# Performance work log

Measured on AMD Instinct MI355X. Metric: run time of the kernel, lower is better.

## Reference

```python
import jax, jax.numpy as jnp
import numpy as np

# GraphConvolutionSparse forward:
#   x = sparse_dropout(X)            (dropout=0.0 -> identity, kept faithful)
#   h = X @ W                        (sparse-dense matmul via segment_sum)
#   h = A @ h                        (sparse-dense matmul via segment_sum)
#   out = relu(h)

DROPOUT = 0.0  # layer default; keep_prob = 1 - dropout

def setup_inputs() -> dict:
    key = jax.random.key(0)
    k1, k2, k3, k4, k5, k6, k7 = jax.random.split(key, 7)
    N = 100000       # nodes
    D_IN = 512       # input feature dim
    D_OUT = 128      # output feature dim
    NNZ_X = 800000   # nonzeros in sparse feature matrix
    N_E = 1600000    # adjacency nonzeros (edges)
    x_vals = jax.random.normal(k1, (NNZ_X,), dtype=jnp.float32)
    x_rows = jax.random.randint(k2, (NNZ_X,), 0, N, dtype=jnp.int32)
    x_cols = jax.random.randint(k3, (NNZ_X,), 0, D_IN, dtype=jnp.int32)
    adj_vals = jax.random.uniform(k4, (N_E,), dtype=jnp.float32)
    adj_rows = jax.random.randint(k5, (N_E,), 0, N, dtype=jnp.int32)
    adj_cols = jax.random.randint(k6, (N_E,), 0, N, dtype=jnp.int32)
    init_range = np.sqrt(6.0 / (D_IN + D_OUT)).astype(np.float32)
    W = jax.random.uniform(k7, (D_IN, D_OUT), minval=-init_range, maxval=init_range, dtype=jnp.float32)
    return {"x_vals": x_vals, "x_rows": x_rows, "x_cols": x_cols,
            "adj_vals": adj_vals, "adj_rows": adj_rows, "adj_cols": adj_cols,
            "W": W, "n_nodes": N}

def reference(x_vals, x_rows, x_cols, adj_vals, adj_rows, adj_cols, W, n_nodes):
    keep_prob = 1.0 - DROPOUT
    # sparse dropout: with dropout=0.0 the mask keeps all entries and scale is 1,
    # so it reduces to the deterministic identity (faithful to tf semantics).
    vals = x_vals * (1.0 / keep_prob)
    # h = X @ W : gather weight rows by feature column, scale, scatter-add by node row
    xw = jax.ops.segment_sum(vals[:, None] * W[x_cols], x_rows, num_segments=n_nodes)  # [N, D_OUT]
    # out = A @ h : gather source-node rows, scale by edge weight, scatter-add to dest
    agg = jax.ops.segment_sum(adj_vals[:, None] * xw[adj_cols], adj_rows, num_segments=n_nodes)  # [N, D_OUT]
    return jax.nn.relu(agg)
```

## Files before the change

kernel.cpp:

```cpp
#include <hip/hip_runtime.h>
#include <hip/hip_fp16.h>


#define DOUT 128
#define RB 32
#define RB_BITS 5
#define NBMAX 4096
#define CAPL 1024
#define COLMASK 131071
#define CTH 256
#define CWAVES 4
#define CAPX 448
#define CAPA 768

static inline size_t align_up(size_t x, size_t a) { return (x + a - 1) & ~(a - 1); }

__device__ inline int wave_incl_scan(int v, int lane) {
    #pragma unroll
    for (int off = 1; off < 64; off <<= 1) {
        int up = __shfl_up(v, off, 64);
        if (lane >= off) v += up;
    }
    return v;
}

__global__ __launch_bounds__(256) void prep_kernel(int* __restrict__ cnts, int ncnt,
                                                   const float* __restrict__ W,
                                                   __half2* __restrict__ Wh, int whtot) {
    int i = blockIdx.x * 256 + threadIdx.x;
    if (i < ncnt) cnts[i] = 0;
    if (i < whtot) {
        int c = i >> 6, l = i & 63;
        Wh[i] = __floats2half2_rn(W[(c << 7) + 2 * l], W[(c << 7) + 2 * l + 1]);
    }
}

__global__ __launch_bounds__(256) void hist_coarse(const int* __restrict__ xr, int nx,
                                                   const int* __restrict__ ar, int na,
                                                   int* __restrict__ cx, int* __restrict__ ca) {
    __shared__ int h[2 * NBMAX];
    for (int i = threadIdx.x; i < 2 * NBMAX; i += 256) h[i] = 0;
    __syncthreads();
    int base = blockIdx.x * 4096;
    int tot = nx + na;
    #pragma unroll
    for (int k = 0; k < 16; ++k) {
        int i = base + k * 256 + threadIdx.x;
        if (i < tot) {
            if (i < nx) atomicAdd(&h[xr[i] >> RB_BITS], 1);
            else        atomicAdd(&h[NBMAX + (ar[i - nx] >> RB_BITS)], 1);
        }
    }
    __syncthreads();
    for (int i = threadIdx.x; i < 2 * NBMAX; i += 256) {
        int c = h[i];
        if (c) {
            if (i < NBMAX) atomicAdd(&cx[i], c);
            else           atomicAdd(&ca[i - NBMAX], c);
        }
    }
}

__global__ __launch_bounds__(1024) void scan_nb(const int* __restrict__ cx, const int* __restrict__ ca,
                                                int* __restrict__ bx, int* __restrict__ ba,
                                                int* __restrict__ curx, int* __restrict__ cura, int nb) {
    const int* c = blockIdx.x ? ca : cx;
    int* bs  = blockIdx.x ? ba : bx;
    int* cur = blockIdx.x ? cura : curx;
    __shared__ int wsum[16];
    __shared__ int woff[16];
    __shared__ int carry_s, chunk_tot;
    int tid = threadIdx.x, lane = tid & 63, wid = tid >> 6;
    if (tid == 0) carry_s = 0;
    __syncthreads();
    for (int base = 0; base < nb; base += 1024) {
        int i = base + tid;
        int v = (i < nb) ? c[i] : 0;
        int incl = wave_incl_scan(v, lane);
        if (lane == 63) wsum[wid] = incl;
        __syncthreads();
        if (wid == 0 && lane < 16) {
            int s = wsum[lane];
            int is = s;
            #pragma unroll
            for (int off = 1; off < 16; off <<= 1) {
                int up = __shfl_up(is, off, 64);
                if (lane >= off) is += up;
            }
            woff[lane] = is - s;
            if (lane == 15) chunk_tot = is;
        }
        __syncthreads();
        int excl = incl - v + woff[wid] + carry_s;
        if (i < nb) { bs[i] = excl; cur[i] = excl; }
        __syncthreads();
        if (tid == 0) carry_s += chunk_tot;
        __syncthreads();
    }
    if (tid == 0) bs[nb] = carry_s;
}

__global__ __launch_bounds__(512) void bucket_scatter2(const int* __restrict__ xr, const int* __restrict__ xc,
                                                       const float* __restrict__ xv, int nx,
                                                       const int* __restrict__ ar, const int* __restrict__ ac,
                                                       const float* __restrict__ av, int na,
                                                       int* __restrict__ curx, int* __restrict__ cura,
                                                       int2* __restrict__ stx, int2* __restrict__ sta,
                                                       int nb, int nblk_x, int capx, int capa) {
    const int* rows; const int* cols; const float* vals; int n;
    int* gcur; int2* stage; int base; int cap;
    if (blockIdx.x < nblk_x) {
        rows = xr; cols = xc; vals = xv; n = nx; gcur = curx; stage = stx;
        base = blockIdx.x * 4096; cap = capx;
    } else {
        rows = ar; cols = ac; vals = av; n = na; gcur = cura; stage = sta;
        base = (blockIdx.x - nblk_x) * 4096; cap = capa;
    }
    __shared__ int h[NBMAX];
    __shared__ int bcur[NBMAX];
    for (int i = threadIdx.x; i < nb; i += 512) h[i] = 0;
    __syncthreads();
    int rr[8]; int cc[8]; float vv[8];
    #pragma unroll
    for (int k = 0; k < 8; ++k) {
        int i = base + k * 512 + threadIdx.x;
        rr[k] = -1;
        if (i < n) {
            rr[k] = rows[i]; cc[k] = cols[i]; vv[k] = vals[i];
            atomicAdd(&h[rr[k] >> RB_BITS], 1);
        }
    }
    __syncthreads();
    for (int b = threadIdx.x; b < nb; b += 512) {
        int c = h[b];
        if (c) {
            int r = atomicAdd(&gcur[b], c);
            bcur[b] = (cap > 0) ? (b * cap + r) : r;
        }
    }
    __syncthreads();
    #pragma unroll
    for (int k = 0; k < 8; ++k) {
        if (rr[k] >= 0) {
            int b = rr[k] >> RB_BITS;
            int p = atomicAdd(&bcur[b], 1);
            if (cap == 0 || p < b * cap + cap)
                stage[p] = make_int2(((rr[k] & (RB - 1)) << 17) | cc[k], __float_as_int(vv[k]));
        }
    }
}


__global__ __launch_bounds__(CTH) void consumer_xw(const int* __restrict__ bx, const int* __restrict__ gcnt,
                                                   const int2* __restrict__ stage,
                                                   const __half2* __restrict__ Wh, __half2* __restrict__ xwh,
                                                   int N, int cap) {
    __shared__ int2 sp[CAPL];
    __shared__ int hoff[RB + 1];
    __shared__ int curs[RB];
    int b = blockIdx.x;
    int s, cnt;
    if (cap > 0) { s = b * cap; cnt = min(gcnt[b], cap); }
    else         { s = bx[b]; cnt = bx[b + 1] - s; }
    int tid = threadIdx.x, lane = tid & 63, wid = tid >> 6;
    bool fast = (cnt <= CAPL);
    if (tid < RB) curs[tid] = 0;
    __syncthreads();
    if (fast) {
        for (int i = tid; i < cnt; i += CTH)
            atomicAdd(&curs[(stage[s + i].x >> 17) & (RB - 1)], 1);
    }
    __syncthreads();
    if (wid == 0) {
        int v = (lane < RB) ? curs[lane] : 0;
        int incl = wave_incl_scan(v, lane);
        if (lane < RB) {
            int excl = incl - v;
            hoff[lane] = excl;
            curs[lane] = excl;
            if (lane == RB - 1) hoff[RB] = incl;
        }
    }
    __syncthreads();
    if (fast) {
        for (int i = tid; i < cnt; i += CTH) {
            int2 p = stage[s + i];
            int r = (p.x >> 17) & (RB - 1);
            sp[atomicAdd(&curs[r], 1)] = p;
        }
    }
    __syncthreads();
    int row0 = b << RB_BITS;
    #pragma unroll 1
    for (int rr = 0; rr < RB / CWAVES; ++rr) {
        int r = wid + rr * CWAVES;
        int grow = row0 + r;
        if (grow >= N) continue;
        float ax = 0.f, ay = 0.f;
        if (fast) {
            int j = hoff[r], o1 = hoff[r + 1];
            for (; j + 3 < o1; j += 4) {
                int2 c0 = sp[j], c1 = sp[j + 1], c2 = sp[j + 2], c3 = sp[j + 3];
                float2 w0 = __half22float2(Wh[((size_t)(c0.x & COLMASK) << 6) + lane]);
                float2 w1 = __half22float2(Wh[((size_t)(c1.x & COLMASK) << 6) + lane]);
                float2 w2 = __half22float2(Wh[((size_t)(c2.x & COLMASK) << 6) + lane]);
                float2 w3 = __half22float2(Wh[((size_t)(c3.x & COLMASK) << 6) + lane]);
                float v0 = __int_as_float(c0.y), v1 = __int_as_float(c1.y);
                float v2 = __int_as_float(c2.y), v3 = __int_as_float(c3.y);
                ax += v0 * w0.x + v1 * w1.x + v2 * w2.x + v3 * w3.x;
                ay += v0 * w0.y + v1 * w1.y + v2 * w2.y + v3 * w3.y;
            }
            for (; j < o1; ++j) {
                int2 c0 = sp[j];
                float2 w0 = __half22float2(Wh[((size_t)(c0.x & COLMASK) << 6) + lane]);
                float v0 = __int_as_float(c0.y);
                ax += v0 * w0.x; ay += v0 * w0.y;
            }
        } else {
            for (int j = 0; j < cnt; ++j) {
                int2 c0 = stage[s + j];
                if (((c0.x >> 17) & (RB - 1)) == r) {
                    float2 w0 = __half22float2(Wh[((size_t)(c0.x & COLMASK) << 6) + lane]);
                    float v0 = __int_as_float(c0.y);
                    ax += v0 * w0.x; ay += v0 * w0.y;
                }
            }
        }
        xwh[((size_t)grow << 6) + lane] = __float22half2_rn(make_float2(ax, ay));
    }
}

__global__ __launch_bounds__(CTH) void consumer_adj(const int* __restrict__ ba, const int* __restrict__ gcnt,
                                                    const int2* __restrict__ stage,
                                                    const __half2* __restrict__ xwh, float* __restrict__ out,
                                                    int N, int cap) {
    __shared__ int2 sp[CAPL];
    __shared__ int hoff[RB + 1];
    __shared__ int curs[RB];
    int b = blockIdx.x;
    int s, cnt;
    if (cap > 0) { s = b * cap; cnt = min(gcnt[b], cap); }
    else         { s = ba[b]; cnt = ba[b + 1] - s; }
    int tid = threadIdx.x, lane = tid & 63, wid = tid >> 6;
    bool fast = (cnt <= CAPL);
    if (tid < RB) curs[tid] = 0;
    __syncthreads();
    if (fast) {
        for (int i = tid; i < cnt; i += CTH)
            atomicAdd(&curs[(stage[s + i].x >> 17) & (RB - 1)], 1);
    }
    __syncthreads();
    if (wid == 0) {
        int v = (lane < RB) ? curs[lane] : 0;
        int incl = wave_incl_scan(v, lane);
        if (lane < RB) {
            int excl = incl - v;
            hoff[lane] = excl;
            curs[lane] = excl;
            if (lane == RB - 1) hoff[RB] = incl;
        }
    }
    __syncthreads();
    if (fast) {
        for (int i = tid; i < cnt; i += CTH) {
            int2 p = stage[s + i];
            int r = (p.x >> 17) & (RB - 1);
            sp[atomicAdd(&curs[r], 1)] = p;
        }
    }
    __syncthreads();
    int row0 = b << RB_BITS;
    #pragma unroll 1
    for (int rr = 0; rr < RB / CWAVES; ++rr) {
        int r = wid + rr * CWAVES;
        int grow = row0 + r;
        if (grow >= N) continue;
        float ax = 0.f, ay = 0.f;
        if (fast) {
            int j = hoff[r], o1 = hoff[r + 1];
            for (; j + 3 < o1; j += 4) {
                int2 c0 = sp[j], c1 = sp[j + 1], c2 = sp[j + 2], c3 = sp[j + 3];
                float2 h0 = __half22float2(xwh[((size_t)(c0.x & COLMASK) << 6) + lane]);
                float2 h1 = __half22float2(xwh[((size_t)(c1.x & COLMASK) << 6) + lane]);
                float2 h2 = __half22float2(xwh[((size_t)(c2.x & COLMASK) << 6) + lane]);
                float2 h3 = __half22float2(xwh[((size_t)(c3.x & COLMASK) << 6) + lane]);
                float v0 = __int_as_float(c0.y), v1 = __int_as_float(c1.y);
                float v2 = __int_as_float(c2.y), v3 = __int_as_float(c3.y);
                ax += v0 * h0.x + v1 * h1.x + v2 * h2.x + v3 * h3.x;
                ay += v0 * h0.y + v1 * h1.y + v2 * h2.y + v3 * h3.y;
            }
            for (; j < o1; ++j) {
                int2 c0 = sp[j];
                float2 h0 = __half22float2(xwh[((size_t)(c0.x & COLMASK) << 6) + lane]);
                float v0 = __int_as_float(c0.y);
                ax += v0 * h0.x; ay += v0 * h0.y;
            }
        } else {
            for (int j = 0; j < cnt; ++j) {
                int2 c0 = stage[s + j];
                if (((c0.x >> 17) & (RB - 1)) == r) {
                    float2 h0 = __half22float2(xwh[((size_t)(c0.x & COLMASK) << 6) + lane]);
                    float v0 = __int_as_float(c0.y);
                    ax += v0 * h0.x; ay += v0 * h0.y;
                }
            }
        }
        ((float2*)(out + (size_t)grow * DOUT))[lane] = make_float2(fmaxf(ax, 0.f), fmaxf(ay, 0.f));
    }
}

__global__ void spmm_xw_atomic(const float* __restrict__ x_vals, const int* __restrict__ x_rows,
                               const int* __restrict__ x_cols, const float* __restrict__ W,
                               float* __restrict__ xw, int nnz) {
    long long t = (long long)blockIdx.x * blockDim.x + threadIdx.x;
    int i = (int)(t >> 7), d = (int)(t & 127);
    if (i >= nnz) return;
    atomicAdd(&xw[(long long)x_rows[i] * DOUT + d], x_vals[i] * W[(long long)x_cols[i] * DOUT + d]);
}
__global__ void spmm_adj_atomic(const float* __restrict__ adj_vals, const int* __restrict__ adj_rows,
                                const int* __restrict__ adj_cols, const float* __restrict__ xw,
                                float* __restrict__ out, int n_e) {
    long long t = (long long)blockIdx.x * blockDim.x + threadIdx.x;
    int e = (int)(t >> 7), d = (int)(t & 127);
    if (e >= n_e) return;
    atomicAdd(&out[(long long)adj_rows[e] * DOUT + d], adj_vals[e] * xw[(long long)adj_cols[e] * DOUT + d]);
}
__global__ void relu_kernel(float4* __restrict__ out, int n4) {
    int i = blockIdx.x * blockDim.x + threadIdx.x;
    if (i >= n4) return;
    float4 v = out[i];
    v.x = fmaxf(v.x, 0.f); v.y = fmaxf(v.y, 0.f);
    v.z = fmaxf(v.z, 0.f); v.w = fmaxf(v.w, 0.f);
    out[i] = v;
}

extern "C" void kernel_launch(void* const* d_in, const int* in_sizes, int n_in,
                              void* d_out, int out_size, void* d_ws, size_t ws_size,
                              hipStream_t stream) {
    const float* x_vals   = (const float*)d_in[0];
    const int*   x_rows   = (const int*)d_in[1];
    const int*   x_cols   = (const int*)d_in[2];
    const float* adj_vals = (const float*)d_in[3];
    const int*   adj_rows = (const int*)d_in[4];
    const int*   adj_cols = (const int*)d_in[5];
    const float* W        = (const float*)d_in[6];
    float* out = (float*)d_out;

    const int nnz_x = in_sizes[0];
    const int n_e   = in_sizes[3];
    const int N     = out_size / DOUT;
    const int D_IN  = in_sizes[6] / DOUT;
    const int nb    = (N + RB - 1) / RB;

    char* ws = (char*)d_ws;
    size_t off = 0;
    size_t xw_off   = off; off = align_up(off + (size_t)N * DOUT * sizeof(__half), 128);
    size_t wh_off   = off; off = align_up(off + (size_t)D_IN * 64 * sizeof(__half2), 128);
    size_t cx_off   = off; off += (size_t)NBMAX * sizeof(int);
    size_t ca_off   = off; off = align_up(off + (size_t)NBMAX * sizeof(int), 128);
    size_t bx_off   = off; off = align_up(off + (size_t)(NBMAX + 1) * sizeof(int), 128);
    size_t baoff    = off; off = align_up(off + (size_t)(NBMAX + 1) * sizeof(int), 128);
    size_t head = off;
    size_t sxc_off = head;
    size_t sac_off = align_up(sxc_off + (size_t)nb * CAPX * sizeof(int2), 128);
    size_t needed_cap = align_up(sac_off + (size_t)nb * CAPA * sizeof(int2), 128);
    size_t sxm_off = head;
    size_t sam_off = align_up(sxm_off + (size_t)nnz_x * sizeof(int2), 128);
    size_t needed_mid = align_up(sam_off + (size_t)n_e * sizeof(int2), 128);

    bool ok_dims = (nb <= NBMAX) && (N <= (COLMASK + 1));
    const int ncnt = 2 * NBMAX;
    const int whtot = D_IN * 64;
    const int prep_n = (ncnt > whtot ? ncnt : whtot);

    if (ok_dims && ws_size >= needed_cap) {
        __half2* xwh  = (__half2*)(ws + xw_off);
        __half2* Wh   = (__half2*)(ws + wh_off);
        int*  cx      = (int*)(ws + cx_off);
        int*  ca      = (int*)(ws + ca_off);
        int2* stage_x = (int2*)(ws + sxc_off);
        int2* stage_a = (int2*)(ws + sac_off);

        prep_kernel<<<(prep_n + 255) / 256, 256, 0, stream>>>(cx, ncnt, W, Wh, whtot);

        int nblk_x = (nnz_x + 4095) / 4096;
        int nblk_a = (n_e + 4095) / 4096;
        bucket_scatter2<<<nblk_x + nblk_a, 512, 0, stream>>>(x_rows, x_cols, x_vals, nnz_x,
                                                             adj_rows, adj_cols, adj_vals, n_e,
                                                             cx, ca, stage_x, stage_a,
                                                             nb, nblk_x, CAPX, CAPA);
        consumer_xw<<<nb, CTH, 0, stream>>>(nullptr, cx, stage_x, Wh, xwh, N, CAPX);
        consumer_adj<<<nb, CTH, 0, stream>>>(nullptr, ca, stage_a, xwh, out, N, CAPA);
    } else if (ok_dims && ws_size >= needed_mid) {
        __half2* xwh  = (__half2*)(ws + xw_off);
        __half2* Wh   = (__half2*)(ws + wh_off);
        int*  cx      = (int*)(ws + cx_off);
        int*  ca      = (int*)(ws + ca_off);
        int*  bx      = (int*)(ws + bx_off);
        int*  ba      = (int*)(ws + baoff);
        int2* stage_x = (int2*)(ws + sxm_off);
        int2* stage_a = (int2*)(ws + sam_off);

        prep_kernel<<<(prep_n + 255) / 256, 256, 0, stream>>>(cx, ncnt, W, Wh, whtot);

        int tot = nnz_x + n_e;
        hist_coarse<<<(tot + 4095) / 4096, 256, 0, stream>>>(x_rows, nnz_x, adj_rows, n_e, cx, ca);
        scan_nb<<<2, 1024, 0, stream>>>(cx, ca, bx, ba, cx, ca, nb);

        int nblk_x = (nnz_x + 4095) / 4096;
        int nblk_a = (n_e + 4095) / 4096;
        bucket_scatter2<<<nblk_x + nblk_a, 512, 0, stream>>>(x_rows, x_cols, x_vals, nnz_x,
                                                             adj_rows, adj_cols, adj_vals, n_e,
                                                             cx, ca, stage_x, stage_a,
                                                             nb, nblk_x, 0, 0);
        consumer_xw<<<nb, CTH, 0, stream>>>(bx, nullptr, stage_x, Wh, xwh, N, 0);
        consumer_adj<<<nb, CTH, 0, stream>>>(ba, nullptr, stage_a, xwh, out, N, 0);
    } else {
        float* xw = (float*)ws;
        hipMemsetAsync(xw, 0, (size_t)out_size * sizeof(float), stream);
        hipMemsetAsync(out, 0, (size_t)out_size * sizeof(float), stream);
        long long t1 = (long long)nnz_x * DOUT;
        spmm_xw_atomic<<<(int)((t1 + 255) / 256), 256, 0, stream>>>(x_vals, x_rows, x_cols, W, xw, nnz_x);
        long long t2 = (long long)n_e * DOUT;
        spmm_adj_atomic<<<(int)((t2 + 255) / 256), 256, 0, stream>>>(adj_vals, adj_rows, adj_cols, xw, out, n_e);
        relu_kernel<<<(out_size / 4 + 255) / 256, 256, 0, stream>>>((float4*)out, out_size / 4);
    }
}
```

Baseline: 216.3 us.

## Chunk adjacency gathers by source-column range across rows for cache locality

The adjacency consumer now buckets staged edges by (row, column-chunk) using bits above the row field, giving 256 bins. Each wave processes its 8 rows chunk-by-chunk, so all waves sweep similar source-column ranges at the same time, which is meant to improve L2 reuse of gathered xw rows. Staged entries are also held in registers between the counting and scatter passes in both consumers instead of being reloaded, and occupancy hints are added to the launch bounds. The row mapping changes from interleaved to contiguous per wave, and keeping 8 float2 accumulators raises register pressure.

```diff
diff --git a/kernel.cpp b/kernel.cpp
--- a/kernel.cpp
+++ b/kernel.cpp
@@ -5,6 +5,8 @@
 #define DOUT 128
 #define RB 32
 #define RB_BITS 5
+#define NCH 8
+#define KMAX (RB * NCH)
 #define NBMAX 4096
 #define CAPL 1024
 #define COLMASK 131071
@@ -151,10 +153,10 @@
 }
 
 
-__global__ __launch_bounds__(CTH) void consumer_xw(const int* __restrict__ bx, const int* __restrict__ gcnt,
-                                                   const int2* __restrict__ stage,
-                                                   const __half2* __restrict__ Wh, __half2* __restrict__ xwh,
-                                                   int N, int cap) {
+__global__ __launch_bounds__(CTH, 8) void consumer_xw(const int* __restrict__ bx, const int* __restrict__ gcnt,
+                                                      const int2* __restrict__ stage,
+                                                      const __half2* __restrict__ Wh, __half2* __restrict__ xwh,
+                                                      int N, int cap) {
     __shared__ int2 sp[CAPL];
     __shared__ int hoff[RB + 1];
     __shared__ int curs[RB];
@@ -166,9 +168,16 @@
     bool fast = (cnt <= CAPL);
     if (tid < RB) curs[tid] = 0;
     __syncthreads();
+    int2 pr[4];
     if (fast) {
-        for (int i = tid; i < cnt; i += CTH)
-            atomicAdd(&curs[(stage[s + i].x >> 17) & (RB - 1)], 1);
+        #pragma unroll
+        for (int k = 0; k < 4; ++k) {
+            int i = k * CTH + tid;
+            if (i < cnt) {
+                pr[k] = stage[s + i];
+                atomicAdd(&curs[(pr[k].x >> 17) & (RB - 1)], 1);
+            }
+        }
     }
     __syncthreads();
     if (wid == 0) {
@@ -183,10 +192,13 @@
     }
     __syncthreads();
     if (fast) {
-        for (int i = tid; i < cnt; i += CTH) {
-            int2 p = stage[s + i];
-            int r = (p.x >> 17) & (RB - 1);
-            sp[atomicAdd(&curs[r], 1)] = p;
+        #pragma unroll
+        for (int k = 0; k < 4; ++k) {
+            int i = k * CTH + tid;
+            if (i < cnt) {
+                int r = (pr[k].x >> 17) & (RB - 1);
+                sp[atomicAdd(&curs[r], 1)] = pr[k];
+            }
         }
     }
     __syncthreads();
@@ -230,72 +242,102 @@
     }
 }
 
-__global__ __launch_bounds__(CTH) void consumer_adj(const int* __restrict__ ba, const int* __restrict__ gcnt,
-                                                    const int2* __restrict__ stage,
-                                                    const __half2* __restrict__ xwh, float* __restrict__ out,
-                                                    int N, int cap) {
+__global__ __launch_bounds__(CTH, 8) void consumer_adj(const int* __restrict__ ba, const int* __restrict__ gcnt,
+                                                       const int2* __restrict__ stage,
+                                                       const __half2* __restrict__ xwh, float* __restrict__ out,
+                                                       int N, int cap) {
     __shared__ int2 sp[CAPL];
-    __shared__ int hoff[RB + 1];
-    __shared__ int curs[RB];
+    __shared__ int off[KMAX + 1];
+    __shared__ int curs[KMAX];
     int b = blockIdx.x;
     int s, cnt;
     if (cap > 0) { s = b * cap; cnt = min(gcnt[b], cap); }
     else         { s = ba[b]; cnt = ba[b + 1] - s; }
     int tid = threadIdx.x, lane = tid & 63, wid = tid >> 6;
     bool fast = (cnt <= CAPL);
-    if (tid < RB) curs[tid] = 0;
-    __syncthreads();
+    if (tid < KMAX) curs[tid] = 0;
+    __syncthreads();
+    int2 pr[4];
     if (fast) {
-        for (int i = tid; i < cnt; i += CTH)
-            atomicAdd(&curs[(stage[s + i].x >> 17) & (RB - 1)], 1);
+        #pragma unroll
+        for (int k = 0; k < 4; ++k) {
+            int i = k * CTH + tid;
+            if (i < cnt) {
+                pr[k] = stage[s + i];
+                atomicAdd(&curs[(pr[k].x >> 14) & (KMAX - 1)], 1);
+            }
+        }
     }
     __syncthreads();
     if (wid == 0) {
-        int v = (lane < RB) ? curs[lane] : 0;
-        int incl = wave_incl_scan(v, lane);
-        if (lane < RB) {
-            int excl = incl - v;
-            hoff[lane] = excl;
-            curs[lane] = excl;
-            if (lane == RB - 1) hoff[RB] = incl;
-        }
+        int carry = 0;
+        #pragma unroll
+        for (int q = 0; q < 4; ++q) {
+            int k = (q << 6) + lane;
+            int v = curs[k];
+            int incl = wave_incl_scan(v, lane) + carry;
+            off[k] = incl - v;
+            curs[k] = incl - v;
+            carry = __shfl(incl, 63, 64);
+        }
+        if (lane == 0) off[KMAX] = carry;
     }
     __syncthreads();
     if (fast) {
-        for (int i = tid; i < cnt; i += CTH) {
-            int2 p = stage[s + i];
-            int r = (p.x >> 17) & (RB - 1);
-            sp[atomicAdd(&curs[r], 1)] = p;
+        #pragma unroll
+        for (int k = 0; k < 4; ++k) {
+            int i = k * CTH + tid;
+            if (i < cnt)
+                sp[atomicAdd(&curs[(pr[k].x >> 14) & (KMAX - 1)], 1)] = pr[k];
         }
     }
     __syncthreads();
     int row0 = b << RB_BITS;
-    #pragma unroll 1
-    for (int rr = 0; rr < RB / CWAVES; ++rr) {
-        int r = wid + rr * CWAVES;
-        int grow = row0 + r;
-        if (grow >= N) continue;
-        float ax = 0.f, ay = 0.f;
-        if (fast) {
-            int j = hoff[r], o1 = hoff[r + 1];
-            for (; j + 3 < o1; j += 4) {
-                int2 c0 = sp[j], c1 = sp[j + 1], c2 = sp[j + 2], c3 = sp[j + 3];
-                float2 h0 = __half22float2(xwh[((size_t)(c0.x & COLMASK) << 6) + lane]);
-                float2 h1 = __half22float2(xwh[((size_t)(c1.x & COLMASK) << 6) + lane]);
-                float2 h2 = __half22float2(xwh[((size_t)(c2.x & COLMASK) << 6) + lane]);
-                float2 h3 = __half22float2(xwh[((size_t)(c3.x & COLMASK) << 6) + lane]);
-                float v0 = __int_as_float(c0.y), v1 = __int_as_float(c1.y);
-                float v2 = __int_as_float(c2.y), v3 = __int_as_float(c3.y);
-                ax += v0 * h0.x + v1 * h1.x + v2 * h2.x + v3 * h3.x;
-                ay += v0 * h0.y + v1 * h1.y + v2 * h2.y + v3 * h3.y;
-            }
-            for (; j < o1; ++j) {
-                int2 c0 = sp[j];
-                float2 h0 = __half22float2(xwh[((size_t)(c0.x & COLMASK) << 6) + lane]);
-                float v0 = __int_as_float(c0.y);
-                ax += v0 * h0.x; ay += v0 * h0.y;
-            }
-        } else {
+    if (fast) {
+        float2 acc[8];
+        #pragma unroll
+        for (int rr = 0; rr < 8; ++rr) acc[rr] = make_float2(0.f, 0.f);
+        #pragma unroll 1
+        for (int ch = 0; ch < NCH; ++ch) {
+            #pragma unroll
+            for (int rr = 0; rr < 8; ++rr) {
+                int base = ((((wid << 3) + rr) << 3) + ch);
+                int j = off[base], o1 = off[base + 1];
+                float ax = acc[rr].x, ay = acc[rr].y;
+                for (; j + 3 < o1; j += 4) {
+                    int2 c0 = sp[j], c1 = sp[j + 1], c2 = sp[j + 2], c3 = sp[j + 3];
+                    float2 h0 = __half22float2(xwh[((size_t)(c0.x & COLMASK) << 6) + lane]);
+                    float2 h1 = __half22float2(xwh[((size_t)(c1.x & COLMASK) << 6) + lane]);
+                    float2 h2 = __half22float2(xwh[((size_t)(c2.x & COLMASK) << 6) + lane]);
+                    float2 h3 = __half22float2(xwh[((size_t)(c3.x & COLMASK) << 6) + lane]);
+                    float v0 = __int_as_float(c0.y), v1 = __int_as_float(c1.y);
+                    float v2 = __int_as_float(c2.y), v3 = __int_as_float(c3.y);
+                    ax += v0 * h0.x + v1 * h1.x + v2 * h2.x + v3 * h3.x;
+                    ay += v0 * h0.y + v1 * h1.y + v2 * h2.y + v3 * h3.y;
+                }
+                for (; j < o1; ++j) {
+                    int2 c0 = sp[j];
+                    float2 h0 = __half22float2(xwh[((size_t)(c0.x & COLMASK) << 6) + lane]);
+                    float v0 = __int_as_float(c0.y);
+                    ax += v0 * h0.x; ay += v0 * h0.y;
+                }
+                acc[rr].x = ax; acc[rr].y = ay;
+            }
+        }
+        #pragma unroll
+        for (int rr = 0; rr < 8; ++rr) {
+            int grow = row0 + (wid << 3) + rr;
+            if (grow < N)
+                ((float2*)(out + (size_t)grow * DOUT))[lane] =
+                    make_float2(fmaxf(acc[rr].x, 0.f), fmaxf(acc[rr].y, 0.f));
+        }
+    } else {
+        #pragma unroll 1
+        for (int rr = 0; rr < RB / CWAVES; ++rr) {
+            int r = wid + rr * CWAVES;
+            int grow = row0 + r;
+            if (grow >= N) continue;
+            float ax = 0.f, ay = 0.f;
             for (int j = 0; j < cnt; ++j) {
                 int2 c0 = stage[s + j];
                 if (((c0.x >> 17) & (RB - 1)) == r) {
@@ -304,8 +346,8 @@
                     ax += v0 * h0.x; ay += v0 * h0.y;
                 }
             }
-        }
-        ((float2*)(out + (size_t)grow * DOUT))[lane] = make_float2(fmaxf(ax, 0.f), fmaxf(ay, 0.f));
+            ((float2*)(out + (size_t)grow * DOUT))[lane] = make_float2(fmaxf(ax, 0.f), fmaxf(ay, 0.f));
+        }
     }
 }
 
```

New measurement: 242.3 us. +12.0%, slower.
